# Optimization experiments

Measured on AMD Instinct MI355X. Metric: run time of the kernel, lower is better.

The kernel has to match this reference:

```python
import jax, jax.numpy as jnp
import numpy as np


def setup_inputs() -> dict:
    key = jax.random.key(0)
    k1, k2 = jax.random.split(key)
    N, L, C = 64, 256, 384
    x = jax.random.normal(k1, (N, L, C), dtype=jnp.float32)
    # frame counts per phoneme, 1..16
    durations = jax.random.randint(k2, (N, L), 1, 17, dtype=jnp.int32)
    # expand_max_len = max over batch of total duration (static Python int)
    mel_max_length = int(jnp.max(jnp.sum(durations, axis=-1)))
    return {"x": x, "durations": durations, "mel_max_length": mel_max_length}


def reference(x, durations, mel_max_length):
    # Equivalent to: alignment[n, t, j] = 1 if starts[n,j] <= t < csum[n,j];
    # output = alignment @ x. Implemented as a direct gather via cumulative
    # durations (searchsorted), avoiding the O(N*T*L) one-hot matmul.
    N, L, C = x.shape
    csum = jnp.cumsum(durations, axis=-1)            # [N, L] exclusive end per phoneme
    t = jnp.arange(mel_max_length)                   # [T]
    # source phoneme index for each output frame: first j with t < csum[j]
    idx = jax.vmap(lambda c: jnp.searchsorted(c, t, side='right'))(csum)  # [N, T]
    total = csum[:, -1]                              # [N] total frames per example
    valid = t[None, :] < total[:, None]              # [N, T]
    idx = jnp.minimum(idx, L - 1)
    out = jnp.take_along_axis(x, idx[..., None], axis=1)   # [N, T, C]
    out = jnp.where(valid[..., None], out, jnp.zeros((), dtype=x.dtype))
    mel_pos = jnp.arange(1, mel_max_length + 1, dtype=jnp.int64)[None, :]  # [1, T]
    return out, mel_pos
```

## Files before the change

kernel.cpp:

```cpp
#include <hip/hip_runtime.h>

#define N_B    64
#define L_IN   256
#define C_DIM  384
#define C4     (C_DIM / 4)
#define F4_PER_BLOCK 2048
#define ITERS  (F4_PER_BLOCK / 256)

typedef float vfloat4 __attribute__((ext_vector_type(4)));

__global__ __launch_bounds__(256) void lr_fused_kernel(const vfloat4* __restrict__ x,
                                                       const int* __restrict__ dur,
                                                       vfloat4* __restrict__ out,
                                                       float* __restrict__ melpos,
                                                       int melmax) {
    __shared__ int csum[L_IN];
    __shared__ int r_tab[32];

    const int n      = blockIdx.x & 63;
    const int bchunk = blockIdx.x >> 6;
    const int tid    = (int)threadIdx.x;
    const int row_f4 = melmax * C4;
    const int start  = bchunk * F4_PER_BLOCK;
    if (start >= row_f4) return;
    const bool full  = (start + F4_PER_BLOCK) <= row_f4;
    const int end    = full ? (start + F4_PER_BLOCK) : row_f4;

    csum[tid] = dur[n * L_IN + tid];
    __syncthreads();
    #pragma unroll
    for (int off = 1; off < L_IN; off <<= 1) {
        int add = (tid >= off) ? csum[tid - off] : 0;
        __syncthreads();
        csum[tid] += add;
        __syncthreads();
    }
    const int total = csum[L_IN - 1];

    const int t0    = start / C4;
    const int tlast = (end - 1) / C4;
    const int tcnt  = tlast - t0 + 1;
    if (tid < tcnt) {
        const int t = t0 + tid;
        int r = -1;
        if (t < total) {
            int lo = 0, hi = L_IN;
            #pragma unroll
            for (int s = 0; s < 8; ++s) {
                int mid = (lo + hi) >> 1;
                if (csum[mid] <= t) lo = mid + 1; else hi = mid;
            }
            r = (lo < (L_IN - 1)) ? lo : (L_IN - 1);
        }
        r_tab[tid] = r;
        if (n == 0) melpos[t] = (float)(t + 1);
    }
    __syncthreads();

    const size_t obase = (size_t)n * row_f4;
    if (full) {
        vfloat4 v[ITERS];
        #pragma unroll
        for (int i = 0; i < ITERS; ++i) {
            const int off = start + tid + 256 * i;
            const int t   = off / C4;
            const int c4  = off - t * C4;
            const int r   = r_tab[t - t0];
            const int rc  = (r >= 0) ? r : 0;
            vfloat4 tmp = x[(n * L_IN + rc) * C4 + c4];
            v[i] = (r >= 0) ? tmp : (vfloat4)0.f;
        }
        #pragma unroll
        for (int i = 0; i < ITERS; ++i) {
            __builtin_nontemporal_store(v[i], &out[obase + start + tid + 256 * i]);
        }
    } else {
        for (int off = start + tid; off < end; off += 256) {
            const int t  = off / C4;
            const int c4 = off - t * C4;
            const int r  = r_tab[t - t0];
            vfloat4 v = (vfloat4)0.f;
            if (r >= 0) v = x[(n * L_IN + r) * C4 + c4];
            __builtin_nontemporal_store(v, &out[obase + off]);
        }
    }
}

extern "C" void kernel_launch(void* const* d_in, const int* in_sizes, int n_in,
                              void* d_out, int out_size, void* d_ws, size_t ws_size,
                              hipStream_t stream) {
    const float* x  = (const float*)d_in[0];
    const int* dur  = (const int*)d_in[1];
    const int melmax = out_size / (N_B * C_DIM + 1);

    const int row_f4 = melmax * C4;
    const int blocks_per_n = (row_f4 + F4_PER_BLOCK - 1) / F4_PER_BLOCK;
    float* mp = (float*)d_out + (size_t)N_B * melmax * C_DIM;

    lr_fused_kernel<<<blocks_per_n * N_B, 256, 0, stream>>>(
        (const vfloat4*)x, dur, (vfloat4*)d_out, mp, melmax);
}
```

Before: 260.7 us.

## Split index computation into separate kernel and remap gather blocks per XCD

The per-block prefix-sum and binary search over durations move out of the gather kernel into a small index kernel that writes frame-to-phoneme indices to the workspace. This way the cumsum runs 256 times instead of once for every output chunk. The gather kernel then loads its indices from that buffer. Block IDs are also remapped so that all chunks of one batch row land on the same XCD, to improve L2 reuse of x rows. The cost is a second kernel launch and a global round trip for the index table.

```diff
diff --git a/kernel.cpp b/kernel.cpp
--- a/kernel.cpp
+++ b/kernel.cpp
@@ -6,25 +6,18 @@
 #define C4     (C_DIM / 4)
 #define F4_PER_BLOCK 2048
 #define ITERS  (F4_PER_BLOCK / 256)
+#define SPLIT  4
 
 typedef float vfloat4 __attribute__((ext_vector_type(4)));
 
-__global__ __launch_bounds__(256) void lr_fused_kernel(const vfloat4* __restrict__ x,
-                                                       const int* __restrict__ dur,
-                                                       vfloat4* __restrict__ out,
-                                                       float* __restrict__ melpos,
-                                                       int melmax) {
+__global__ __launch_bounds__(256) void lr_idx_kernel(const int* __restrict__ dur,
+                                                     int* __restrict__ idx_out,
+                                                     float* __restrict__ melpos,
+                                                     int melmax) {
     __shared__ int csum[L_IN];
-    __shared__ int r_tab[32];
-
-    const int n      = blockIdx.x & 63;
-    const int bchunk = blockIdx.x >> 6;
-    const int tid    = (int)threadIdx.x;
-    const int row_f4 = melmax * C4;
-    const int start  = bchunk * F4_PER_BLOCK;
-    if (start >= row_f4) return;
-    const bool full  = (start + F4_PER_BLOCK) <= row_f4;
-    const int end    = full ? (start + F4_PER_BLOCK) : row_f4;
+    const int n    = blockIdx.x & 63;
+    const int part = blockIdx.x >> 6;
+    const int tid  = (int)threadIdx.x;
 
     csum[tid] = dur[n * L_IN + tid];
     __syncthreads();
@@ -37,11 +30,10 @@
     }
     const int total = csum[L_IN - 1];
 
-    const int t0    = start / C4;
-    const int tlast = (end - 1) / C4;
-    const int tcnt  = tlast - t0 + 1;
-    if (tid < tcnt) {
-        const int t = t0 + tid;
+    const int per  = (melmax + SPLIT - 1) / SPLIT;
+    const int tbeg = part * per;
+    const int tend = min(tbeg + per, melmax);
+    for (int t = tbeg + tid; t < tend; t += 256) {
         int r = -1;
         if (t < total) {
             int lo = 0, hi = L_IN;
@@ -52,9 +44,33 @@
             }
             r = (lo < (L_IN - 1)) ? lo : (L_IN - 1);
         }
-        r_tab[tid] = r;
+        idx_out[n * melmax + t] = r;
         if (n == 0) melpos[t] = (float)(t + 1);
     }
+}
+
+__global__ __launch_bounds__(256) void lr_gather_kernel(const vfloat4* __restrict__ x,
+                                                        const int* __restrict__ idx,
+                                                        vfloat4* __restrict__ out,
+                                                        int melmax, int chunks_per_n) {
+    __shared__ int r_tab[32];
+
+    const int j      = (int)blockIdx.x;
+    const int xcd    = j & 7;
+    const int s      = j >> 3;
+    const int n      = xcd + 8 * (s / chunks_per_n);
+    const int bchunk = s % chunks_per_n;
+    const int tid    = (int)threadIdx.x;
+
+    const int row_f4 = melmax * C4;
+    const int start  = bchunk * F4_PER_BLOCK;
+    if (start >= row_f4) return;
+    const bool full  = (start + F4_PER_BLOCK) <= row_f4;
+    const int end    = full ? (start + F4_PER_BLOCK) : row_f4;
+
+    const int t0   = start / C4;
+    const int tcnt = (end - 1) / C4 - t0 + 1;
+    if (tid < tcnt) r_tab[tid] = idx[n * melmax + t0 + tid];
     __syncthreads();
 
     const size_t obase = (size_t)n * row_f4;
@@ -93,10 +109,13 @@
     const int* dur  = (const int*)d_in[1];
     const int melmax = out_size / (N_B * C_DIM + 1);
 
+    int* idxbuf = (int*)d_ws;
+    float* mp   = (float*)d_out + (size_t)N_B * melmax * C_DIM;
+
+    lr_idx_kernel<<<N_B * SPLIT, 256, 0, stream>>>(dur, idxbuf, mp, melmax);
+
     const int row_f4 = melmax * C4;
-    const int blocks_per_n = (row_f4 + F4_PER_BLOCK - 1) / F4_PER_BLOCK;
-    float* mp = (float*)d_out + (size_t)N_B * melmax * C_DIM;
-
-    lr_fused_kernel<<<blocks_per_n * N_B, 256, 0, stream>>>(
-        (const vfloat4*)x, dur, (vfloat4*)d_out, mp, melmax);
+    const int chunks_per_n = (row_f4 + F4_PER_BLOCK - 1) / F4_PER_BLOCK;
+    lr_gather_kernel<<<chunks_per_n * N_B, 256, 0, stream>>>(
+        (const vfloat4*)x, idxbuf, (vfloat4*)d_out, melmax, chunks_per_n);
 }
```

New measurement: 257.3 us. About the same (-1.3%).
